# Kernel optimization log

Measured on AMD Instinct MI355X. Metric: run time of the kernel, lower is better.

Reference implementation:

```python
import jax, jax.numpy as jnp
import numpy as np

N = 1048576          # nodes at current depth (children), divisible by 8
M = N // 8           # non-empty parent nodes (conv outputs)
NNUM_PARENT = 262144 # total parent nodes at depth-1
C_IN = 128
C_OUT = 256


def setup_inputs() -> dict:
    key = jax.random.key(0)
    k1, k2, k3 = jax.random.split(key, 3)
    data = jax.random.normal(k1, (N, C_IN), dtype=jnp.float32)
    weights = jax.random.normal(k2, (8, C_IN, C_OUT), dtype=jnp.float32) * (1.0 / np.sqrt(8 * C_IN))
    # sorted unique positions of non-empty parents within [0, NNUM_PARENT)
    perm = jax.random.permutation(k3, NNUM_PARENT)
    nempty_idx = jnp.sort(perm[:M]).astype(jnp.int32)
    return {"data": data, "weights": weights, "nempty_idx": nempty_idx,
            "nnum_parent": NNUM_PARENT}


def reference(data, weights, nempty_idx, nnum_parent):
    # kernel-2 stride-2 conv: each consecutive group of 8 children -> one parent
    c_in, c_out = weights.shape[1], weights.shape[2]
    out = data.reshape(-1, 8 * c_in) @ weights.reshape(8 * c_in, c_out)  # [M, C_out]
    # octree_pad at depth-1: scatter into all parent nodes, zeros at empty ones
    full = jnp.zeros((nnum_parent, c_out), dtype=out.dtype).at[nempty_idx].set(out)
    return full
```

## Files before the change

### kernel.cpp

```cpp
#include <hip/hip_runtime.h>
#include <hip/hip_bf16.h>

typedef float f32x4 __attribute__((ext_vector_type(4)));
typedef short s16x8 __attribute__((ext_vector_type(8)));

using bf16 = __hip_bfloat16;

namespace {
constexpr int KD = 1024;
constexpr int BM = 128;
constexpr int BK = 32;
constexpr int NT = KD / BK;
constexpr int MBLK = 131072 / BM;
constexpr int ZBLK = 512;
}

typedef __attribute__((address_space(1))) const void GVoid;
typedef __attribute__((address_space(3))) void LVoid;

__device__ __forceinline__ void gld16(const void* g, void* l) {
  __builtin_amdgcn_global_load_lds((GVoid*)g, (LVoid*)l, 16, 0, 0);
}

__device__ __forceinline__ s16x8 cvt8(f32x4 a, f32x4 b) {
  union { s16x8 v; bf16 h[8]; } u;
#pragma unroll
  for (int j = 0; j < 4; ++j) u.h[j] = __float2bfloat16(a[j]);
#pragma unroll
  for (int j = 0; j < 4; ++j) u.h[j + 4] = __float2bfloat16(b[j]);
  return u.v;
}

__global__ void k_transpose_w(const float* __restrict__ w, bf16* __restrict__ bt) {
  int t = blockIdx.x * 256 + threadIdx.x;
  int n = t & 255;
  int k0 = (t >> 8) << 3;
  union { s16x8 v; bf16 h[8]; } u;
#pragma unroll
  for (int j = 0; j < 8; ++j)
    u.h[j] = __float2bfloat16(w[(size_t)(k0 + j) * 256 + n]);
  *(s16x8*)(bt + (size_t)n * KD + k0) = u.v;
}

__global__ void k_clear_flags(int* __restrict__ flags, int np4) {
  int i = blockIdx.x * 256 + threadIdx.x;
  if (i < np4) ((int4*)flags)[i] = make_int4(0, 0, 0, 0);
}

__global__ void k_set_flags(const int* __restrict__ idx, int* __restrict__ flags, int m) {
  int i = blockIdx.x * 256 + threadIdx.x;
  if (i < m) flags[idx[i]] = 1;
}

__global__ __launch_bounds__(512, 2)
void k_fused(const float* __restrict__ A, const bf16* __restrict__ Bt,
             const int* __restrict__ idx, const int* __restrict__ flags,
             float* __restrict__ out, int NP) {
  __shared__ float As[4][BM * BK];
  __shared__ bf16  Bs[4][256 * BK];

  const int tid = threadIdx.x;
  const int lane = tid & 63;
  const int wave = tid >> 6;
  const int bid = blockIdx.x;

  if (bid % 3 == 2) {
    const int zb = bid / 3;
    const f32x4 z = {0.f, 0.f, 0.f, 0.f};
    for (int row = zb * 8 + wave; row < NP; row += ZBLK * 8) {
      if (flags[row] == 0)
        *(f32x4*)(out + (size_t)row * 256 + lane * 4) = z;
    }
    return;
  }

  const int gid = (bid / 3) * 2 + (bid % 3);
  const int m0 = gid * BM;
  const int wm = wave >> 2;
  const int wn = wave & 3;

  const int as0 = tid, as1 = 512 + tid;
  const int ar0 = as0 >> 3, ac0 = (as0 & 7) ^ (ar0 & 6);
  const int ar1 = as1 >> 3, ac1 = (as1 & 7) ^ (ar1 & 6);
  const float* aSrc0 = A + (size_t)(m0 + ar0) * KD + ac0 * 4;
  const float* aSrc1 = A + (size_t)(m0 + ar1) * KD + ac1 * 4;
  const int aOff0 = (wave * 64) * 4;
  const int aOff1 = (512 + wave * 64) * 4;

  const int bs0 = tid, bs1 = 512 + tid;
  const int br0 = bs0 >> 2, bc0 = (bs0 & 3) ^ (br0 & 3);
  const int br1 = bs1 >> 2, bc1 = (bs1 & 3) ^ (br1 & 3);
  const bf16* bSrc0 = Bt + (size_t)br0 * KD + bc0 * 8;
  const bf16* bSrc1 = Bt + (size_t)br1 * KD + bc1 * 8;
  const int bOff0 = (wave * 64) * 8;
  const int bOff1 = (512 + wave * 64) * 8;

  const int arow = wm * 64 + (lane & 15);
  const int kc = lane >> 4;
  const int aRd = arow * 32 + (((2 * kc) ^ (arow & 6)) * 4);
  const int brow = wn * 64 + (lane & 15);
  const int bRd = brow * 32 + ((kc ^ (brow & 3)) * 8);

  f32x4 acc[4][4] = {};

  auto stage = [&](int buf, int t) {
    gld16(aSrc0 + t * BK, &As[buf][aOff0]);
    gld16(aSrc1 + t * BK, &As[buf][aOff1]);
    gld16(bSrc0 + t * BK, &Bs[buf][bOff0]);
    gld16(bSrc1 + t * BK, &Bs[buf][bOff1]);
  };

  stage(0, 0);
  stage(1, 1);
  stage(2, 2);

#pragma unroll 1
  for (int t = 0; t < NT; ++t) {
    if (t + 3 < NT) {
      stage((t + 3) & 3, t + 3);
      asm volatile("s_waitcnt vmcnt(12)" ::: "memory");
    } else if (t + 3 == NT) {
      asm volatile("s_waitcnt vmcnt(8)" ::: "memory");
    } else if (t + 2 == NT) {
      asm volatile("s_waitcnt vmcnt(4)" ::: "memory");
    } else {
      asm volatile("s_waitcnt vmcnt(0)" ::: "memory");
    }
    __builtin_amdgcn_s_barrier();

    const int cur = t & 3;
    s16x8 bfr[4];
#pragma unroll
    for (int fn = 0; fn < 4; ++fn)
      bfr[fn] = *(const s16x8*)(&Bs[cur][bRd + fn * 512]);

#pragma unroll
    for (int fm = 0; fm < 4; ++fm) {
      f32x4 lo = *(const f32x4*)(&As[cur][aRd + fm * 512]);
      f32x4 hi = *(const f32x4*)(&As[cur][aRd + fm * 512 + 4]);
      s16x8 af = cvt8(lo, hi);
#pragma unroll
      for (int fn = 0; fn < 4; ++fn)
        acc[fm][fn] = __builtin_amdgcn_mfma_f32_16x16x32_bf16(
            af, bfr[fn], acc[fm][fn], 0, 0, 0);
    }

    asm volatile("" ::: "memory");
    __builtin_amdgcn_s_barrier();
  }

  const int col0 = wn * 64 + (lane & 15);
  const int rb = m0 + wm * 64 + (kc << 2);
#pragma unroll
  for (int fm = 0; fm < 4; ++fm) {
    const int4 rows = *(const int4*)(idx + rb + fm * 16);
    const int rj[4] = {rows.x, rows.y, rows.z, rows.w};
#pragma unroll
    for (int j = 0; j < 4; ++j) {
      float* op = out + (size_t)rj[j] * 256 + col0;
#pragma unroll
      for (int fn = 0; fn < 4; ++fn)
        op[fn * 16] = acc[fm][fn][j];
    }
  }
}

extern "C" void kernel_launch(void* const* d_in, const int* in_sizes, int n_in,
                              void* d_out, int out_size, void* d_ws, size_t ws_size,
                              hipStream_t stream) {
  const float* data = (const float*)d_in[0];
  const float* w    = (const float*)d_in[1];
  const int*   idx  = (const int*)d_in[2];
  float* out = (float*)d_out;

  const int M  = in_sizes[2];
  const int NP = out_size / 256;

  int* flags = (int*)d_ws;
  bf16* bt = (bf16*)((char*)d_ws + (size_t)NP * sizeof(int));

  k_transpose_w<<<128, 256, 0, stream>>>(w, bt);
  k_clear_flags<<<(NP / 4 + 255) / 256, 256, 0, stream>>>(flags, NP / 4);
  k_set_flags<<<(M + 255) / 256, 256, 0, stream>>>(idx, flags, M);
  k_fused<<<MBLK + ZBLK, 512, 0, stream>>>(data, bt, idx, flags, out, NP);
}
```

Measured before the change: 283.4 us.

## Load B fragments directly from global into registers, drop the B LDS stage

The transposed bf16 weight tile is no longer staged through shared memory. Each wave now reads its B fragments straight from global memory (expected to hit in cache) at the top of every K step. Only the A tile uses the 4-deep LDS ring, so the trailing per-iteration barrier is removed and the vmcnt waits are recomputed. LDS use per block halves and launch bounds ask for 4 blocks per CU to raise occupancy. The cost is more global traffic per wave for B, and tighter register limits that may cause spills given the 64-float accumulator.

```diff
diff --git a/kernel.cpp b/kernel.cpp
--- a/kernel.cpp
+++ b/kernel.cpp
@@ -52,12 +52,11 @@
   if (i < m) flags[idx[i]] = 1;
 }
 
-__global__ __launch_bounds__(512, 2)
+__global__ __launch_bounds__(512, 4)
 void k_fused(const float* __restrict__ A, const bf16* __restrict__ Bt,
              const int* __restrict__ idx, const int* __restrict__ flags,
              float* __restrict__ out, int NP) {
   __shared__ float As[4][BM * BK];
-  __shared__ bf16  Bs[4][256 * BK];
 
   const int tid = threadIdx.x;
   const int lane = tid & 63;
@@ -87,27 +86,22 @@
   const int aOff0 = (wave * 64) * 4;
   const int aOff1 = (512 + wave * 64) * 4;
 
-  const int bs0 = tid, bs1 = 512 + tid;
-  const int br0 = bs0 >> 2, bc0 = (bs0 & 3) ^ (br0 & 3);
-  const int br1 = bs1 >> 2, bc1 = (bs1 & 3) ^ (br1 & 3);
-  const bf16* bSrc0 = Bt + (size_t)br0 * KD + bc0 * 8;
-  const bf16* bSrc1 = Bt + (size_t)br1 * KD + bc1 * 8;
-  const int bOff0 = (wave * 64) * 8;
-  const int bOff1 = (512 + wave * 64) * 8;
+  const int r = lane & 15;
+  const int kc = lane >> 4;
 
-  const int arow = wm * 64 + (lane & 15);
-  const int kc = lane >> 4;
+  const int arow = wm * 64 + r;
   const int aRd = arow * 32 + (((2 * kc) ^ (arow & 6)) * 4);
-  const int brow = wn * 64 + (lane & 15);
-  const int bRd = brow * 32 + ((kc ^ (brow & 3)) * 8);
+
+  const bf16* bp0 = Bt + (size_t)(wn * 64 + r) * KD + kc * 8;
+  const bf16* bp1 = bp0 + (size_t)16 * KD;
+  const bf16* bp2 = bp0 + (size_t)32 * KD;
+  const bf16* bp3 = bp0 + (size_t)48 * KD;
 
   f32x4 acc[4][4] = {};
 
   auto stage = [&](int buf, int t) {
     gld16(aSrc0 + t * BK, &As[buf][aOff0]);
     gld16(aSrc1 + t * BK, &As[buf][aOff1]);
-    gld16(bSrc0 + t * BK, &Bs[buf][bOff0]);
-    gld16(bSrc1 + t * BK, &Bs[buf][bOff1]);
   };
 
   stage(0, 0);
@@ -116,40 +110,37 @@
 
 #pragma unroll 1
   for (int t = 0; t < NT; ++t) {
-    if (t + 3 < NT) {
-      stage((t + 3) & 3, t + 3);
+    if (t >= 2 && t < NT - 2) {
       asm volatile("s_waitcnt vmcnt(12)" ::: "memory");
-    } else if (t + 3 == NT) {
+    } else if (t == 1) {
       asm volatile("s_waitcnt vmcnt(8)" ::: "memory");
-    } else if (t + 2 == NT) {
+    } else {
       asm volatile("s_waitcnt vmcnt(4)" ::: "memory");
-    } else {
-      asm volatile("s_waitcnt vmcnt(0)" ::: "memory");
     }
     __builtin_amdgcn_s_barrier();
 
+    s16x8 bfr0 = *(const s16x8*)(bp0 + t * BK);
+    s16x8 bfr1 = *(const s16x8*)(bp1 + t * BK);
+    s16x8 bfr2 = *(const s16x8*)(bp2 + t * BK);
+    s16x8 bfr3 = *(const s16x8*)(bp3 + t * BK);
+    asm volatile("" ::: "memory");
+
+    if (t + 3 < NT) stage((t + 3) & 3, t + 3);
+
     const int cur = t & 3;
-    s16x8 bfr[4];
-#pragma unroll
-    for (int fn = 0; fn < 4; ++fn)
-      bfr[fn] = *(const s16x8*)(&Bs[cur][bRd + fn * 512]);
-
 #pragma unroll
     for (int fm = 0; fm < 4; ++fm) {
       f32x4 lo = *(const f32x4*)(&As[cur][aRd + fm * 512]);
       f32x4 hi = *(const f32x4*)(&As[cur][aRd + fm * 512 + 4]);
       s16x8 af = cvt8(lo, hi);
-#pragma unroll
-      for (int fn = 0; fn < 4; ++fn)
-        acc[fm][fn] = __builtin_amdgcn_mfma_f32_16x16x32_bf16(
-            af, bfr[fn], acc[fm][fn], 0, 0, 0);
+      acc[fm][0] = __builtin_amdgcn_mfma_f32_16x16x32_bf16(af, bfr0, acc[fm][0], 0, 0, 0);
+      acc[fm][1] = __builtin_amdgcn_mfma_f32_16x16x32_bf16(af, bfr1, acc[fm][1], 0, 0, 0);
+      acc[fm][2] = __builtin_amdgcn_mfma_f32_16x16x32_bf16(af, bfr2, acc[fm][2], 0, 0, 0);
+      acc[fm][3] = __builtin_amdgcn_mfma_f32_16x16x32_bf16(af, bfr3, acc[fm][3], 0, 0, 0);
     }
-
-    asm volatile("" ::: "memory");
-    __builtin_amdgcn_s_barrier();
   }
 
-  const int col0 = wn * 64 + (lane & 15);
+  const int col0 = wn * 64 + r;
   const int rb = m0 + wm * 64 + (kc << 2);
 #pragma unroll
   for (int fm = 0; fm < 4; ++fm) {
```

After: 290.4 us. +2.5%, slower.
